# Kernel optimization log

Hardware: AMD Instinct MI355X
Metric: run time of the kernel (lower is better)

## Reference

```python
import jax, jax.numpy as jnp
import numpy as np

B, T, F, H, O = 16384, 128, 9, 128, 12


def setup_inputs() -> dict:
    key = jax.random.key(0)
    ks = jax.random.split(key, 14)
    s = 1.0 / np.sqrt(H)
    u = lambda k, shp: jax.random.uniform(k, shp, jnp.float32, -s, s)
    return {
        "x": jax.random.normal(ks[0], (B, T, F), jnp.float32),
        "W_in": u(ks[1], (H, F)), "b_in": u(ks[2], (H,)),
        "Wih0": u(ks[3], (4 * H, H)), "Whh0": u(ks[4], (4 * H, H)),
        "bih0": u(ks[5], (4 * H,)), "bhh0": u(ks[6], (4 * H,)),
        "Wih1": u(ks[7], (4 * H, H)), "Whh1": u(ks[8], (4 * H, H)),
        "bih1": u(ks[9], (4 * H,)), "bhh1": u(ks[10], (4 * H,)),
        "W_out": u(ks[11], (O, H)), "b_out": u(ks[12], (O,)),
    }


def _cell(h, c, xp, Wih, Whh, bih, bhh):
    # PyTorch LSTM gate order: i, f, g, o
    g = xp @ Wih.T + bih + h @ Whh.T + bhh  # [B, 4H]
    i, f, gg, o = jnp.split(g, 4, axis=-1)
    c = jax.nn.sigmoid(f) * c + jax.nn.sigmoid(i) * jnp.tanh(gg)
    h = jax.nn.sigmoid(o) * jnp.tanh(c)
    return h, c


def reference(x, W_in, b_in, Wih0, Whh0, bih0, bhh0, Wih1, Whh1, bih1, bhh1, W_out, b_out):
    # input projection, all timesteps at once: [B, T, H] -> scan over time
    xp = jnp.einsum('btf,hf->tbh', x, W_in) + b_in
    b = x.shape[0]
    zeros = jnp.zeros((b, H), x.dtype)
    carry0 = (zeros, zeros, zeros, zeros)  # h0, c0, h1, c1

    def step(carry, xt):
        h0, c0, h1, c1 = carry
        h0, c0 = _cell(h0, c0, xt, Wih0, Whh0, bih0, bhh0)
        h1, c1 = _cell(h1, c1, h0, Wih1, Whh1, bih1, bhh1)
        return (h0, c0, h1, c1), None

    (h0, c0, h1, c1), _ = jax.lax.scan(step, carry0, xp)
    # torch forward returns only the LAST step's output: out(h1) with softmax over dim=1
    return jax.nn.softmax(h1 @ W_out.T + b_out, axis=1)
```

## Files before the change

kernel.cpp:

```cpp
#include <hip/hip_runtime.h>
#include <hip/hip_bf16.h>
#include <stdint.h>
#include <stddef.h>

#define T_STEPS 128
#define F_IN 9
#define HID 128
#define OUT_N 12
#define XROW (T_STEPS * F_IN)
#define BATCH 16384

typedef __attribute__((ext_vector_type(8))) short bf16x8;
typedef __attribute__((ext_vector_type(4))) float f32x4;

#define MFMA16(a, b, c) __builtin_amdgcn_mfma_f32_16x16x32_bf16((a), (b), (c), 0, 0, 0)

__device__ __forceinline__ short f2bf(float f) {
  union { float f; uint32_t u; } v; v.f = f;
  return (short)((v.u + 0x7fffu + ((v.u >> 16) & 1u)) >> 16);
}
__device__ __forceinline__ short f2bf_hw(float f) {
  __hip_bfloat16 h = __float2bfloat16(f);
  union { __hip_bfloat16 h; short s; } u; u.h = h;
  return u.s;
}
__device__ __forceinline__ float frcp(float x) { return __builtin_amdgcn_rcpf(x); }
__device__ __forceinline__ float fexp2(float x) { return __builtin_amdgcn_exp2f(x); }
__device__ __forceinline__ float tanh_f(float x) {
  return 1.0f - 2.0f * frcp(1.0f + fexp2(2.8853900817779268f * x));
}

__global__ void prep_x(const float* __restrict__ x, short* __restrict__ xbf) {
  int idx = blockIdx.x * blockDim.x + threadIdx.x;
  int row = idx & (BATCH - 1), t = idx >> 14;
  const float* xp = x + (size_t)row * XROW + t * F_IN;
  short v[16];
#pragma unroll
  for (int j = 0; j < F_IN; ++j) v[j] = f2bf(xp[j]);
#pragma unroll
  for (int j = F_IN; j < 16; ++j) v[j] = 0;
  int4* dst = (int4*)(xbf + (size_t)idx * 16);
  dst[0] = ((const int4*)v)[0];
  dst[1] = ((const int4*)v)[1];
}

__global__ void prep_w0x(const float* __restrict__ W_in, const float* __restrict__ b_in,
                         const float* __restrict__ Wih0, const float* __restrict__ bih0,
                         const float* __restrict__ bhh0, const float* __restrict__ bih1,
                         const float* __restrict__ bhh1,
                         short* __restrict__ w0xf, float* __restrict__ b0x, float* __restrict__ b1) {
  int tid = threadIdx.x;
  int nt = tid >> 4, hl = tid & 15;
  int w = nt >> 2, g = nt & 3;
  int n = g * 128 + w * 16 + hl;
  float wacc[F_IN];
#pragma unroll
  for (int f = 0; f < F_IN; ++f) wacc[f] = 0.f;
  float bacc = 0.f;
  for (int h = 0; h < HID; ++h) {
    float wv = Wih0[n * HID + h];
    bacc += wv * b_in[h];
#pragma unroll
    for (int f = 0; f < F_IN; ++f) wacc[f] += wv * W_in[h * F_IN + f];
  }
  b0x[n] = bacc + bih0[n] + bhh0[n];
  b1[n] = bih1[n] + bhh1[n];
#pragma unroll
  for (int k = 0; k < 32; ++k) {
    int quad = k >> 3, j = k & 7;
    w0xf[((w * 4 + g) * 64 + quad * 16 + hl) * 8 + j] = (k < F_IN) ? f2bf(wacc[k]) : (short)0;
  }
}

__global__ void prep_wrec(const float* __restrict__ Whh0, const float* __restrict__ Wih1,
                          const float* __restrict__ Whh1,
                          short* __restrict__ whh0f, short* __restrict__ w1f) {
  int gt = blockIdx.x * blockDim.x + threadIdx.x;
  if (gt < 2048) {
    int kt = gt >> 9, rr = gt & 511;
    int nt = rr >> 4, hl = rr & 15;
    int w = nt >> 2, g = nt & 3;
    int n = g * 128 + w * 16 + hl;
#pragma unroll
    for (int k = 0; k < 32; ++k) {
      int quad = k >> 3, j = k & 7;
      whh0f[((w * 16 + kt * 4 + g) * 64 + quad * 16 + hl) * 8 + j] =
          f2bf(Whh0[n * HID + kt * 32 + k]);
    }
  } else {
    int g2 = gt - 2048;
    int kt = g2 >> 9, rr = g2 & 511;
    int nt = rr >> 4, hl = rr & 15;
    int w = nt >> 2, g = nt & 3;
    int n = g * 128 + w * 16 + hl;
#pragma unroll
    for (int k = 0; k < 32; ++k) {
      int quad = k >> 3, j = k & 7;
      int kg = kt * 32 + k;
      float v = (kg < HID) ? Wih1[n * HID + kg] : Whh1[n * HID + kg - HID];
      w1f[((w * 32 + kt * 4 + g) * 64 + quad * 16 + hl) * 8 + j] = f2bf(v);
    }
  }
}

__device__ __forceinline__ void lstm_step(
    int t, const short* __restrict__ xpl, const short* __restrict__ wp0,
    const short* __restrict__ wph, const short* __restrict__ wp1,
    const float* sb0, const float* sb1, float* c0, float* c1,
    const short* h0r, short* h0w, const short* h1r, short* h1w,
    int lane, int wr_off, int quad) {
  const f32x4 z4 = {0.f, 0.f, 0.f, 0.f};
  const short* xt = xpl + (size_t)t * 262144;
  bf16x8 xf[2];
#pragma unroll
  for (int mt = 0; mt < 2; ++mt) {
    bf16x8 v = {0, 0, 0, 0, 0, 0, 0, 0};
    if (quad < 2) v = *(const bf16x8*)(xt + mt * 256);
    xf[mt] = v;
  }
  f32x4 acc1[2][4];
  {
    const short* wb = wp1;
    bf16x8 b0_ = *(const bf16x8*)(wb);
    bf16x8 b1_ = *(const bf16x8*)(wb + 512);
    bf16x8 b2_ = *(const bf16x8*)(wb + 1024);
    bf16x8 b3_ = *(const bf16x8*)(wb + 1536);
#pragma unroll
    for (int mt = 0; mt < 2; ++mt) {
      bf16x8 af = *(const bf16x8*)(h0r + ((mt * 4 + 0) * 64 + lane) * 8);
      acc1[mt][0] = MFMA16(af, b0_, z4);
      acc1[mt][1] = MFMA16(af, b1_, z4);
      acc1[mt][2] = MFMA16(af, b2_, z4);
      acc1[mt][3] = MFMA16(af, b3_, z4);
    }
  }
#pragma clang loop unroll_count(3)
  for (int kt = 1; kt < 4; ++kt) {
    const short* wb = wp1 + kt * 2048;
    bf16x8 b0_ = *(const bf16x8*)(wb);
    bf16x8 b1_ = *(const bf16x8*)(wb + 512);
    bf16x8 b2_ = *(const bf16x8*)(wb + 1024);
    bf16x8 b3_ = *(const bf16x8*)(wb + 1536);
#pragma unroll
    for (int mt = 0; mt < 2; ++mt) {
      bf16x8 af = *(const bf16x8*)(h0r + ((mt * 4 + kt) * 64 + lane) * 8);
      acc1[mt][0] = MFMA16(af, b0_, acc1[mt][0]);
      acc1[mt][1] = MFMA16(af, b1_, acc1[mt][1]);
      acc1[mt][2] = MFMA16(af, b2_, acc1[mt][2]);
      acc1[mt][3] = MFMA16(af, b3_, acc1[mt][3]);
    }
  }
#pragma clang loop unroll_count(2)
  for (int kt = 0; kt < 4; ++kt) {
    const short* wb = wp1 + (kt + 4) * 2048;
    bf16x8 b0_ = *(const bf16x8*)(wb);
    bf16x8 b1_ = *(const bf16x8*)(wb + 512);
    bf16x8 b2_ = *(const bf16x8*)(wb + 1024);
    bf16x8 b3_ = *(const bf16x8*)(wb + 1536);
#pragma unroll
    for (int mt = 0; mt < 2; ++mt) {
      bf16x8 af = *(const bf16x8*)(h1r + ((mt * 4 + kt) * 64 + lane) * 8);
      acc1[mt][0] = MFMA16(af, b0_, acc1[mt][0]);
      acc1[mt][1] = MFMA16(af, b1_, acc1[mt][1]);
      acc1[mt][2] = MFMA16(af, b2_, acc1[mt][2]);
      acc1[mt][3] = MFMA16(af, b3_, acc1[mt][3]);
    }
  }
#pragma unroll
  for (int mt = 0; mt < 2; ++mt)
#pragma unroll
    for (int r = 0; r < 4; ++r) {
      float gi = frcp(1.0f + fexp2(fmaf(-1.4426950408889634f, acc1[mt][0][r], sb1[0])));
      float gf = frcp(1.0f + fexp2(fmaf(-1.4426950408889634f, acc1[mt][1][r], sb1[1])));
      float gg = 1.0f - 2.0f * frcp(1.0f + fexp2(fmaf(2.8853900817779268f, acc1[mt][2][r], sb1[2])));
      float go = frcp(1.0f + fexp2(fmaf(-1.4426950408889634f, acc1[mt][3][r], sb1[3])));
      float cn = gf * c1[mt * 4 + r] + gi * gg;
      c1[mt * 4 + r] = cn;
      float hn = go * tanh_f(cn);
      h1w[mt * 2048 + r * 8 + wr_off] = f2bf_hw(hn);
    }
  f32x4 acc0[2][4];
  {
    bf16x8 b0_ = *(const bf16x8*)(wp0);
    bf16x8 b1_ = *(const bf16x8*)(wp0 + 512);
    bf16x8 b2_ = *(const bf16x8*)(wp0 + 1024);
    bf16x8 b3_ = *(const bf16x8*)(wp0 + 1536);
#pragma unroll
    for (int mt = 0; mt < 2; ++mt) {
      acc0[mt][0] = MFMA16(xf[mt], b0_, z4);
      acc0[mt][1] = MFMA16(xf[mt], b1_, z4);
      acc0[mt][2] = MFMA16(xf[mt], b2_, z4);
      acc0[mt][3] = MFMA16(xf[mt], b3_, z4);
    }
  }
#pragma clang loop unroll_count(2)
  for (int kt = 0; kt < 4; ++kt) {
    const short* wb = wph + kt * 2048;
    bf16x8 b0_ = *(const bf16x8*)(wb);
    bf16x8 b1_ = *(const bf16x8*)(wb + 512);
    bf16x8 b2_ = *(const bf16x8*)(wb + 1024);
    bf16x8 b3_ = *(const bf16x8*)(wb + 1536);
#pragma unroll
    for (int mt = 0; mt < 2; ++mt) {
      bf16x8 af = *(const bf16x8*)(h0r + ((mt * 4 + kt) * 64 + lane) * 8);
      acc0[mt][0] = MFMA16(af, b0_, acc0[mt][0]);
      acc0[mt][1] = MFMA16(af, b1_, acc0[mt][1]);
      acc0[mt][2] = MFMA16(af, b2_, acc0[mt][2]);
      acc0[mt][3] = MFMA16(af, b3_, acc0[mt][3]);
    }
  }
#pragma unroll
  for (int mt = 0; mt < 2; ++mt)
#pragma unroll
    for (int r = 0; r < 4; ++r) {
      float gi = frcp(1.0f + fexp2(fmaf(-1.4426950408889634f, acc0[mt][0][r], sb0[0])));
      float gf = frcp(1.0f + fexp2(fmaf(-1.4426950408889634f, acc0[mt][1][r], sb0[1])));
      float gg = 1.0f - 2.0f * frcp(1.0f + fexp2(fmaf(2.8853900817779268f, acc0[mt][2][r], sb0[2])));
      float go = frcp(1.0f + fexp2(fmaf(-1.4426950408889634f, acc0[mt][3][r], sb0[3])));
      float cn = gf * c0[mt * 4 + r] + gi * gg;
      c0[mt * 4 + r] = cn;
      float hn = go * tanh_f(cn);
      h0w[mt * 2048 + r * 8 + wr_off] = f2bf_hw(hn);
    }
  __syncthreads();
}

__global__ void __launch_bounds__(512)
lstm_main(const short* __restrict__ xbf, const short* __restrict__ w0xf,
          const short* __restrict__ whh0f, const short* __restrict__ w1f,
          const float* __restrict__ b0x, const float* __restrict__ b1,
          const float* __restrict__ Wout, const float* __restrict__ bout,
          float* __restrict__ out) {
  __shared__ short h0a[4096], h0b[4096], h1a[4096], h1b[4096];
  __shared__ float h1fp[32 * HID];
  __shared__ float lg[32 * OUT_N];
  __shared__ int gov[2688];

  const int tid = threadIdx.x;
  const int w = tid >> 6, lane = tid & 63;
  const int quad = lane >> 4, c = lane & 15;
  const int rowbase = blockIdx.x * 32;

  {
    for (int i = tid; i < 2048; i += 512) {
      ((int*)h0a)[i] = 0; ((int*)h0b)[i] = 0; ((int*)h1a)[i] = 0; ((int*)h1b)[i] = 0;
    }
    if (tid < 64) ((volatile int*)gov)[tid] = 0;
  }

  const short* wp0 = w0xf + (w * 4) * 512 + lane * 8;
  const short* wph = whh0f + (w * 16) * 512 + lane * 8;
  const short* wp1 = w1f + (w * 32) * 512 + lane * 8;

  const short* xpl = xbf + ((size_t)(rowbase + c) << 4) + ((quad & 1) << 3);

  float sb0[4], sb1[4];
#pragma unroll
  for (int g = 0; g < 4; ++g) {
    int n = g * 128 + w * 16 + c;
    float bv0 = b0x[n], bv1 = b1[n];
    sb0[g] = (g == 2) ? 2.8853900817779268f * bv0 : -1.4426950408889634f * bv0;
    sb1[g] = (g == 2) ? 2.8853900817779268f * bv1 : -1.4426950408889634f * bv1;
  }

  const int kt_w = w >> 1;
  const int klocal = ((w & 1) << 4) + c;
  const int quadA = klocal >> 3;
  const int jA = klocal & 7;
  const int wr_off = (kt_w * 64 + quadA * 16 + quad * 4) * 8 + jA;

  float c0[8], c1[8];
#pragma unroll
  for (int i = 0; i < 8; ++i) { c0[i] = 0.f; c1[i] = 0.f; }

  const f32x4 z4 = {0.f, 0.f, 0.f, 0.f};

  __syncthreads();

  {
    bf16x8 xf[2];
#pragma unroll
    for (int mt = 0; mt < 2; ++mt) {
      bf16x8 v = {0, 0, 0, 0, 0, 0, 0, 0};
      if (quad < 2) v = *(const bf16x8*)(xpl + mt * 256);
      xf[mt] = v;
    }
    f32x4 acc[2][4];
    {
      bf16x8 b0_ = *(const bf16x8*)(wp0);
      bf16x8 b1_ = *(const bf16x8*)(wp0 + 512);
      bf16x8 b2_ = *(const bf16x8*)(wp0 + 1024);
      bf16x8 b3_ = *(const bf16x8*)(wp0 + 1536);
#pragma unroll
      for (int mt = 0; mt < 2; ++mt) {
        acc[mt][0] = MFMA16(xf[mt], b0_, z4);
        acc[mt][1] = MFMA16(xf[mt], b1_, z4);
        acc[mt][2] = MFMA16(xf[mt], b2_, z4);
        acc[mt][3] = MFMA16(xf[mt], b3_, z4);
      }
    }
#pragma unroll
    for (int mt = 0; mt < 2; ++mt)
#pragma unroll
      for (int r = 0; r < 4; ++r) {
        float gi = frcp(1.0f + fexp2(fmaf(-1.4426950408889634f, acc[mt][0][r], sb0[0])));
        float gf = frcp(1.0f + fexp2(fmaf(-1.4426950408889634f, acc[mt][1][r], sb0[1])));
        float gg = 1.0f - 2.0f * frcp(1.0f + fexp2(fmaf(2.8853900817779268f, acc[mt][2][r], sb0[2])));
        float go = frcp(1.0f + fexp2(fmaf(-1.4426950408889634f, acc[mt][3][r], sb0[3])));
        float cn = gi * gg;
        c0[mt * 4 + r] = cn;
        float hn = go * tanh_f(cn);
        h0a[mt * 2048 + r * 8 + wr_off] = f2bf_hw(hn);
      }
  }
  __syncthreads();

#pragma clang loop unroll(disable)
  for (int t = 1; t < 127; t += 2) {
    lstm_step(t,     xpl, wp0, wph, wp1, sb0, sb1, c0, c1, h0a, h0b, h1a, h1b, lane, wr_off, quad);
    lstm_step(t + 1, xpl, wp0, wph, wp1, sb0, sb1, c0, c1, h0b, h0a, h1b, h1a, lane, wr_off, quad);
  }
  lstm_step(127, xpl, wp0, wph, wp1, sb0, sb1, c0, c1, h0a, h0b, h1a, h1b, lane, wr_off, quad);

  {
    f32x4 acc[2][4];
    {
      const short* wb = wp1;
      bf16x8 b0_ = *(const bf16x8*)(wb);
      bf16x8 b1_ = *(const bf16x8*)(wb + 512);
      bf16x8 b2_ = *(const bf16x8*)(wb + 1024);
      bf16x8 b3_ = *(const bf16x8*)(wb + 1536);
#pragma unroll
      for (int mt = 0; mt < 2; ++mt) {
        bf16x8 af = *(const bf16x8*)(h0b + ((mt * 4 + 0) * 64 + lane) * 8);
        acc[mt][0] = MFMA16(af, b0_, z4);
        acc[mt][1] = MFMA16(af, b1_, z4);
        acc[mt][2] = MFMA16(af, b2_, z4);
        acc[mt][3] = MFMA16(af, b3_, z4);
      }
    }
#pragma unroll
    for (int kt = 1; kt < 4; ++kt) {
      const short* wb = wp1 + kt * 2048;
      bf16x8 b0_ = *(const bf16x8*)(wb);
      bf16x8 b1_ = *(const bf16x8*)(wb + 512);
      bf16x8 b2_ = *(const bf16x8*)(wb + 1024);
      bf16x8 b3_ = *(const bf16x8*)(wb + 1536);
#pragma unroll
      for (int mt = 0; mt < 2; ++mt) {
        bf16x8 af = *(const bf16x8*)(h0b + ((mt * 4 + kt) * 64 + lane) * 8);
        acc[mt][0] = MFMA16(af, b0_, acc[mt][0]);
        acc[mt][1] = MFMA16(af, b1_, acc[mt][1]);
        acc[mt][2] = MFMA16(af, b2_, acc[mt][2]);
        acc[mt][3] = MFMA16(af, b3_, acc[mt][3]);
      }
    }
#pragma unroll
    for (int kt = 0; kt < 4; ++kt) {
      const short* wb = wp1 + (kt + 4) * 2048;
      bf16x8 b0_ = *(const bf16x8*)(wb);
      bf16x8 b1_ = *(const bf16x8*)(wb + 512);
      bf16x8 b2_ = *(const bf16x8*)(wb + 1024);
      bf16x8 b3_ = *(const bf16x8*)(wb + 1536);
#pragma unroll
      for (int mt = 0; mt < 2; ++mt) {
        bf16x8 af = *(const bf16x8*)(h1b + ((mt * 4 + kt) * 64 + lane) * 8);
        acc[mt][0] = MFMA16(af, b0_, acc[mt][0]);
        acc[mt][1] = MFMA16(af, b1_, acc[mt][1]);
        acc[mt][2] = MFMA16(af, b2_, acc[mt][2]);
        acc[mt][3] = MFMA16(af, b3_, acc[mt][3]);
      }
    }
#pragma unroll
    for (int mt = 0; mt < 2; ++mt)
#pragma unroll
      for (int r = 0; r < 4; ++r) {
        float gi = frcp(1.0f + fexp2(fmaf(-1.4426950408889634f, acc[mt][0][r], sb1[0])));
        float gf = frcp(1.0f + fexp2(fmaf(-1.4426950408889634f, acc[mt][1][r], sb1[1])));
        float gg = 1.0f - 2.0f * frcp(1.0f + fexp2(fmaf(2.8853900817779268f, acc[mt][2][r], sb1[2])));
        float go = frcp(1.0f + fexp2(fmaf(-1.4426950408889634f, acc[mt][3][r], sb1[3])));
        float cn = gf * c1[mt * 4 + r] + gi * gg;
        float hn = go * tanh_f(cn);
        h1fp[(mt * 16 + quad * 4 + r) * HID + w * 16 + c] = hn;
      }
  }
  __syncthreads();

  {
    int row = tid >> 4, og = tid & 15;
    for (int oc = og; oc < OUT_N; oc += 16) {
      float s = bout[oc];
      const float* wo = Wout + oc * HID;
      const float* hr = h1fp + row * HID;
#pragma unroll 8
      for (int k = 0; k < HID; ++k) s += hr[k] * wo[k];
      lg[row * OUT_N + oc] = s;
    }
  }
  __syncthreads();
  if (tid < 32) {
    int row = tid;
    float m = lg[row * OUT_N];
#pragma unroll
    for (int oc = 1; oc < OUT_N; ++oc) m = fmaxf(m, lg[row * OUT_N + oc]);
    float e[OUT_N];
    float s = 0.f;
#pragma unroll
    for (int oc = 0; oc < OUT_N; ++oc) {
      e[oc] = __expf(lg[row * OUT_N + oc] - m);
      s += e[oc];
    }
    float inv = 1.0f / s;
    float* orow = out + (size_t)(rowbase + row) * OUT_N;
#pragma unroll
    for (int oc = 0; oc < OUT_N; ++oc) orow[oc] = e[oc] * inv;
  }
}

extern "C" void kernel_launch(void* const* d_in, const int* in_sizes, int n_in,
                              void* d_out, int out_size, void* d_ws, size_t ws_size,
                              hipStream_t stream) {
  const float* x    = (const float*)d_in[0];
  const float* W_in = (const float*)d_in[1];
  const float* b_in = (const float*)d_in[2];
  const float* Wih0 = (const float*)d_in[3];
  const float* Whh0 = (const float*)d_in[4];
  const float* bih0 = (const float*)d_in[5];
  const float* bhh0 = (const float*)d_in[6];
  const float* Wih1 = (const float*)d_in[7];
  const float* Whh1 = (const float*)d_in[8];
  const float* bih1 = (const float*)d_in[9];
  const float* bhh1 = (const float*)d_in[10];
  const float* Wout = (const float*)d_in[11];
  const float* bout = (const float*)d_in[12];
  float* out = (float*)d_out;

  short* w0xf  = (short*)d_ws;
  short* whh0f = w0xf + 16384;
  short* w1f   = whh0f + 65536;
  float* b0x   = (float*)(w1f + 131072);
  float* b1    = b0x + 512;
  short* xbf   = (short*)(b1 + 512);

  prep_x<<<(BATCH * T_STEPS) / 256, 256, 0, stream>>>(x, xbf);
  prep_w0x<<<1, 512, 0, stream>>>(W_in, b_in, Wih0, bih0, bhh0, bih1, bhh1, w0xf, b0x, b1);
  prep_wrec<<<12, 512, 0, stream>>>(Whh0, Wih1, Whh1, whh0f, w1f);
  lstm_main<<<512, 512, 0, stream>>>(xbf, w0xf, whh0f, w1f, b0x, b1, Wout, bout, out);
}
```

Measured before the change: 1.212 ms.

## Double rows per block to 64 and move cell state into LDS

Each block now handles 64 batch rows instead of 32 (4 M-tiles per warp), so each recurrent weight fragment loaded per step feeds twice as many MFMAs. The grid is halved to 256 blocks. To hold register pressure down with the larger accumulators, the LSTM cell states c0/c1 move from registers into shared memory and are read and written as float4 per thread each step. The risks are fewer blocks than CUs on the device, more LDS per block, and extra LDS traffic on every step.

```diff
diff --git a/kernel.cpp b/kernel.cpp
--- a/kernel.cpp
+++ b/kernel.cpp
@@ -106,19 +106,13 @@
 __device__ __forceinline__ void lstm_step(
     int t, const short* __restrict__ xpl, const short* __restrict__ wp0,
     const short* __restrict__ wph, const short* __restrict__ wp1,
-    const float* sb0, const float* sb1, float* c0, float* c1,
+    const float* sb0, const float* sb1, float* c0buf, float* c1buf,
     const short* h0r, short* h0w, const short* h1r, short* h1w,
-    int lane, int wr_off, int quad) {
+    int tid, int lane, int wr_off, int quad) {
   const f32x4 z4 = {0.f, 0.f, 0.f, 0.f};
   const short* xt = xpl + (size_t)t * 262144;
-  bf16x8 xf[2];
-#pragma unroll
-  for (int mt = 0; mt < 2; ++mt) {
-    bf16x8 v = {0, 0, 0, 0, 0, 0, 0, 0};
-    if (quad < 2) v = *(const bf16x8*)(xt + mt * 256);
-    xf[mt] = v;
-  }
-  f32x4 acc1[2][4];
+
+  f32x4 acc1[4][4];
   {
     const short* wb = wp1;
     bf16x8 b0_ = *(const bf16x8*)(wb);
@@ -126,7 +120,7 @@
     bf16x8 b2_ = *(const bf16x8*)(wb + 1024);
     bf16x8 b3_ = *(const bf16x8*)(wb + 1536);
 #pragma unroll
-    for (int mt = 0; mt < 2; ++mt) {
+    for (int mt = 0; mt < 4; ++mt) {
       bf16x8 af = *(const bf16x8*)(h0r + ((mt * 4 + 0) * 64 + lane) * 8);
       acc1[mt][0] = MFMA16(af, b0_, z4);
       acc1[mt][1] = MFMA16(af, b1_, z4);
@@ -142,7 +136,7 @@
     bf16x8 b2_ = *(const bf16x8*)(wb + 1024);
     bf16x8 b3_ = *(const bf16x8*)(wb + 1536);
 #pragma unroll
-    for (int mt = 0; mt < 2; ++mt) {
+    for (int mt = 0; mt < 4; ++mt) {
       bf16x8 af = *(const bf16x8*)(h0r + ((mt * 4 + kt) * 64 + lane) * 8);
       acc1[mt][0] = MFMA16(af, b0_, acc1[mt][0]);
       acc1[mt][1] = MFMA16(af, b1_, acc1[mt][1]);
@@ -158,7 +152,7 @@
     bf16x8 b2_ = *(const bf16x8*)(wb + 1024);
     bf16x8 b3_ = *(const bf16x8*)(wb + 1536);
 #pragma unroll
-    for (int mt = 0; mt < 2; ++mt) {
+    for (int mt = 0; mt < 4; ++mt) {
       bf16x8 af = *(const bf16x8*)(h1r + ((mt * 4 + kt) * 64 + lane) * 8);
       acc1[mt][0] = MFMA16(af, b0_, acc1[mt][0]);
       acc1[mt][1] = MFMA16(af, b1_, acc1[mt][1]);
@@ -167,30 +161,35 @@
     }
   }
 #pragma unroll
-  for (int mt = 0; mt < 2; ++mt)
+  for (int mt = 0; mt < 4; ++mt) {
+    f32x4 cp = *(const f32x4*)(c1buf + 4 * (mt * 512 + tid));
+    f32x4 cn;
 #pragma unroll
     for (int r = 0; r < 4; ++r) {
       float gi = frcp(1.0f + fexp2(fmaf(-1.4426950408889634f, acc1[mt][0][r], sb1[0])));
       float gf = frcp(1.0f + fexp2(fmaf(-1.4426950408889634f, acc1[mt][1][r], sb1[1])));
       float gg = 1.0f - 2.0f * frcp(1.0f + fexp2(fmaf(2.8853900817779268f, acc1[mt][2][r], sb1[2])));
       float go = frcp(1.0f + fexp2(fmaf(-1.4426950408889634f, acc1[mt][3][r], sb1[3])));
-      float cn = gf * c1[mt * 4 + r] + gi * gg;
-      c1[mt * 4 + r] = cn;
-      float hn = go * tanh_f(cn);
+      cn[r] = gf * cp[r] + gi * gg;
+      float hn = go * tanh_f(cn[r]);
       h1w[mt * 2048 + r * 8 + wr_off] = f2bf_hw(hn);
     }
-  f32x4 acc0[2][4];
+    *(f32x4*)(c1buf + 4 * (mt * 512 + tid)) = cn;
+  }
+  f32x4 acc0[4][4];
   {
     bf16x8 b0_ = *(const bf16x8*)(wp0);
     bf16x8 b1_ = *(const bf16x8*)(wp0 + 512);
     bf16x8 b2_ = *(const bf16x8*)(wp0 + 1024);
     bf16x8 b3_ = *(const bf16x8*)(wp0 + 1536);
 #pragma unroll
-    for (int mt = 0; mt < 2; ++mt) {
-      acc0[mt][0] = MFMA16(xf[mt], b0_, z4);
-      acc0[mt][1] = MFMA16(xf[mt], b1_, z4);
-      acc0[mt][2] = MFMA16(xf[mt], b2_, z4);
-      acc0[mt][3] = MFMA16(xf[mt], b3_, z4);
+    for (int mt = 0; mt < 4; ++mt) {
+      bf16x8 xf = {0, 0, 0, 0, 0, 0, 0, 0};
+      if (quad < 2) xf = *(const bf16x8*)(xt + mt * 256);
+      acc0[mt][0] = MFMA16(xf, b0_, z4);
+      acc0[mt][1] = MFMA16(xf, b1_, z4);
+      acc0[mt][2] = MFMA16(xf, b2_, z4);
+      acc0[mt][3] = MFMA16(xf, b3_, z4);
     }
   }
 #pragma clang loop unroll_count(2)
@@ -201,7 +200,7 @@
     bf16x8 b2_ = *(const bf16x8*)(wb + 1024);
     bf16x8 b3_ = *(const bf16x8*)(wb + 1536);
 #pragma unroll
-    for (int mt = 0; mt < 2; ++mt) {
+    for (int mt = 0; mt < 4; ++mt) {
       bf16x8 af = *(const bf16x8*)(h0r + ((mt * 4 + kt) * 64 + lane) * 8);
       acc0[mt][0] = MFMA16(af, b0_, acc0[mt][0]);
       acc0[mt][1] = MFMA16(af, b1_, acc0[mt][1]);
@@ -210,18 +209,21 @@
     }
   }
 #pragma unroll
-  for (int mt = 0; mt < 2; ++mt)
+  for (int mt = 0; mt < 4; ++mt) {
+    f32x4 cp = *(const f32x4*)(c0buf + 4 * (mt * 512 + tid));
+    f32x4 cn;
 #pragma unroll
     for (int r = 0; r < 4; ++r) {
       float gi = frcp(1.0f + fexp2(fmaf(-1.4426950408889634f, acc0[mt][0][r], sb0[0])));
       float gf = frcp(1.0f + fexp2(fmaf(-1.4426950408889634f, acc0[mt][1][r], sb0[1])));
       float gg = 1.0f - 2.0f * frcp(1.0f + fexp2(fmaf(2.8853900817779268f, acc0[mt][2][r], sb0[2])));
       float go = frcp(1.0f + fexp2(fmaf(-1.4426950408889634f, acc0[mt][3][r], sb0[3])));
-      float cn = gf * c0[mt * 4 + r] + gi * gg;
-      c0[mt * 4 + r] = cn;
-      float hn = go * tanh_f(cn);
+      cn[r] = gf * cp[r] + gi * gg;
+      float hn = go * tanh_f(cn[r]);
       h0w[mt * 2048 + r * 8 + wr_off] = f2bf_hw(hn);
     }
+    *(f32x4*)(c0buf + 4 * (mt * 512 + tid)) = cn;
+  }
   __syncthreads();
 }
 
@@ -231,21 +233,21 @@
           const float* __restrict__ b0x, const float* __restrict__ b1,
           const float* __restrict__ Wout, const float* __restrict__ bout,
           float* __restrict__ out) {
-  __shared__ short h0a[4096], h0b[4096], h1a[4096], h1b[4096];
-  __shared__ float h1fp[32 * HID];
-  __shared__ float lg[32 * OUT_N];
-  __shared__ int gov[2688];
+  __shared__ short h0a[8192], h0b[8192], h1a[8192], h1b[8192];
+  __shared__ float h1fp_c0[64 * HID];
+  __shared__ float c1buf[64 * HID];
+  __shared__ float lg[64 * OUT_N];
 
   const int tid = threadIdx.x;
   const int w = tid >> 6, lane = tid & 63;
   const int quad = lane >> 4, c = lane & 15;
-  const int rowbase = blockIdx.x * 32;
-
-  {
-    for (int i = tid; i < 2048; i += 512) {
+  const int rowbase = blockIdx.x * 64;
+
+  {
+    for (int i = tid; i < 4096; i += 512) {
       ((int*)h0a)[i] = 0; ((int*)h0b)[i] = 0; ((int*)h1a)[i] = 0; ((int*)h1b)[i] = 0;
     }
-    if (tid < 64) ((volatile int*)gov)[tid] = 0;
+    for (int i = tid; i < 8192; i += 512) { h1fp_c0[i] = 0.f; c1buf[i] = 0.f; }
   }
 
   const short* wp0 = w0xf + (w * 4) * 512 + lane * 8;
@@ -269,61 +271,56 @@
   const int jA = klocal & 7;
   const int wr_off = (kt_w * 64 + quadA * 16 + quad * 4) * 8 + jA;
 
-  float c0[8], c1[8];
-#pragma unroll
-  for (int i = 0; i < 8; ++i) { c0[i] = 0.f; c1[i] = 0.f; }
-
   const f32x4 z4 = {0.f, 0.f, 0.f, 0.f};
 
   __syncthreads();
 
   {
-    bf16x8 xf[2];
-#pragma unroll
-    for (int mt = 0; mt < 2; ++mt) {
-      bf16x8 v = {0, 0, 0, 0, 0, 0, 0, 0};
-      if (quad < 2) v = *(const bf16x8*)(xpl + mt * 256);
-      xf[mt] = v;
-    }
-    f32x4 acc[2][4];
+    f32x4 acc[4][4];
     {
       bf16x8 b0_ = *(const bf16x8*)(wp0);
       bf16x8 b1_ = *(const bf16x8*)(wp0 + 512);
       bf16x8 b2_ = *(const bf16x8*)(wp0 + 1024);
       bf16x8 b3_ = *(const bf16x8*)(wp0 + 1536);
 #pragma unroll
-      for (int mt = 0; mt < 2; ++mt) {
-        acc[mt][0] = MFMA16(xf[mt], b0_, z4);
-        acc[mt][1] = MFMA16(xf[mt], b1_, z4);
-        acc[mt][2] = MFMA16(xf[mt], b2_, z4);
-        acc[mt][3] = MFMA16(xf[mt], b3_, z4);
-      }
-    }
-#pragma unroll
-    for (int mt = 0; mt < 2; ++mt)
+      for (int mt = 0; mt < 4; ++mt) {
+        bf16x8 xf = {0, 0, 0, 0, 0, 0, 0, 0};
+        if (quad < 2) xf = *(const bf16x8*)(xpl + mt * 256);
+        acc[mt][0] = MFMA16(xf, b0_, z4);
+        acc[mt][1] = MFMA16(xf, b1_, z4);
+        acc[mt][2] = MFMA16(xf, b2_, z4);
+        acc[mt][3] = MFMA16(xf, b3_, z4);
+      }
+    }
+#pragma unroll
+    for (int mt = 0; mt < 4; ++mt) {
+      f32x4 cn;
 #pragma unroll
       for (int r = 0; r < 4; ++r) {
         float gi = frcp(1.0f + fexp2(fmaf(-1.4426950408889634f, acc[mt][0][r], sb0[0])));
-        float gf = frcp(1.0f + fexp2(fmaf(-1.4426950408889634f, acc[mt][1][r], sb0[1])));
         float gg = 1.0f - 2.0f * frcp(1.0f + fexp2(fmaf(2.8853900817779268f, acc[mt][2][r], sb0[2])));
         float go = frcp(1.0f + fexp2(fmaf(-1.4426950408889634f, acc[mt][3][r], sb0[3])));
-        float cn = gi * gg;
-        c0[mt * 4 + r] = cn;
-        float hn = go * tanh_f(cn);
+        cn[r] = gi * gg;
+        float hn = go * tanh_f(cn[r]);
         h0a[mt * 2048 + r * 8 + wr_off] = f2bf_hw(hn);
       }
+      *(f32x4*)(h1fp_c0 + 4 * (mt * 512 + tid)) = cn;
+    }
   }
   __syncthreads();
 
 #pragma clang loop unroll(disable)
   for (int t = 1; t < 127; t += 2) {
-    lstm_step(t,     xpl, wp0, wph, wp1, sb0, sb1, c0, c1, h0a, h0b, h1a, h1b, lane, wr_off, quad);
-    lstm_step(t + 1, xpl, wp0, wph, wp1, sb0, sb1, c0, c1, h0b, h0a, h1b, h1a, lane, wr_off, quad);
-  }
-  lstm_step(127, xpl, wp0, wph, wp1, sb0, sb1, c0, c1, h0a, h0b, h1a, h1b, lane, wr_off, quad);
-
-  {
-    f32x4 acc[2][4];
+    lstm_step(t,     xpl, wp0, wph, wp1, sb0, sb1, h1fp_c0, c1buf, h0a, h0b, h1a, h1b,
+              tid, lane, wr_off, quad);
+    lstm_step(t + 1, xpl, wp0, wph, wp1, sb0, sb1, h1fp_c0, c1buf, h0b, h0a, h1b, h1a,
+              tid, lane, wr_off, quad);
+  }
+  lstm_step(127, xpl, wp0, wph, wp1, sb0, sb1, h1fp_c0, c1buf, h0a, h0b, h1a, h1b,
+            tid, lane, wr_off, quad);
+
+  {
+    f32x4 acc[4][4];
     {
       const short* wb = wp1;
       bf16x8 b0_ = *(const bf16x8*)(wb);
@@ -331,7 +328,7 @@
       bf16x8 b2_ = *(const bf16x8*)(wb + 1024);
       bf16x8 b3_ = *(const bf16x8*)(wb + 1536);
 #pragma unroll
-      for (int mt = 0; mt < 2; ++mt) {
+      for (int mt = 0; mt < 4; ++mt) {
         bf16x8 af = *(const bf16x8*)(h0b + ((mt * 4 + 0) * 64 + lane) * 8);
         acc[mt][0] = MFMA16(af, b0_, z4);
         acc[mt][1] = MFMA16(af, b1_, z4);
@@ -347,7 +344,7 @@
       bf16x8 b2_ = *(const bf16x8*)(wb + 1024);
       bf16x8 b3_ = *(const bf16x8*)(wb + 1536);
 #pragma unroll
-      for (int mt = 0; mt < 2; ++mt) {
+      for (int mt = 0; mt < 4; ++mt) {
         bf16x8 af = *(const bf16x8*)(h0b + ((mt * 4 + kt) * 64 + lane) * 8);
         acc[mt][0] = MFMA16(af, b0_, acc[mt][0]);
         acc[mt][1] = MFMA16(af, b1_, acc[mt][1]);
@@ -363,7 +360,7 @@
       bf16x8 b2_ = *(const bf16x8*)(wb + 1024);
       bf16x8 b3_ = *(const bf16x8*)(wb + 1536);
 #pragma unroll
-      for (int mt = 0; mt < 2; ++mt) {
+      for (int mt = 0; mt < 4; ++mt) {
         bf16x8 af = *(const bf16x8*)(h1b + ((mt * 4 + kt) * 64 + lane) * 8);
         acc[mt][0] = MFMA16(af, b0_, acc[mt][0]);
         acc[mt][1] = MFMA16(af, b1_, acc[mt][1]);
@@ -371,34 +368,37 @@
         acc[mt][3] = MFMA16(af, b3_, acc[mt][3]);
       }
     }
-#pragma unroll
-    for (int mt = 0; mt < 2; ++mt)
+    __syncthreads();
+#pragma unroll
+    for (int mt = 0; mt < 4; ++mt) {
+      f32x4 cp = *(const f32x4*)(c1buf + 4 * (mt * 512 + tid));
 #pragma unroll
       for (int r = 0; r < 4; ++r) {
         float gi = frcp(1.0f + fexp2(fmaf(-1.4426950408889634f, acc[mt][0][r], sb1[0])));
         float gf = frcp(1.0f + fexp2(fmaf(-1.4426950408889634f, acc[mt][1][r], sb1[1])));
         float gg = 1.0f - 2.0f * frcp(1.0f + fexp2(fmaf(2.8853900817779268f, acc[mt][2][r], sb1[2])));
         float go = frcp(1.0f + fexp2(fmaf(-1.4426950408889634f, acc[mt][3][r], sb1[3])));
-        float cn = gf * c1[mt * 4 + r] + gi * gg;
+        float cn = gf * cp[r] + gi * gg;
         float hn = go * tanh_f(cn);
-        h1fp[(mt * 16 + quad * 4 + r) * HID + w * 16 + c] = hn;
-      }
+        h1fp_c0[(mt * 16 + quad * 4 + r) * HID + w * 16 + c] = hn;
+      }
+    }
   }
   __syncthreads();
 
   {
-    int row = tid >> 4, og = tid & 15;
-    for (int oc = og; oc < OUT_N; oc += 16) {
+    int row = tid >> 3, og = tid & 7;
+    for (int oc = og; oc < OUT_N; oc += 8) {
       float s = bout[oc];
       const float* wo = Wout + oc * HID;
-      const float* hr = h1fp + row * HID;
+      const float* hr = h1fp_c0 + row * HID;
 #pragma unroll 8
       for (int k = 0; k < HID; ++k) s += hr[k] * wo[k];
       lg[row * OUT_N + oc] = s;
     }
   }
   __syncthreads();
-  if (tid < 32) {
+  if (tid < 64) {
     int row = tid;
     float m = lg[row * OUT_N];
 #pragma unroll
@@ -445,5 +445,5 @@
   prep_x<<<(BATCH * T_STEPS) / 256, 256, 0, stream>>>(x, xbf);
   prep_w0x<<<1, 512, 0, stream>>>(W_in, b_in, Wih0, bih0, bhh0, bih1, bhh1, w0xf, b0x, b1);
   prep_wrec<<<12, 512, 0, stream>>>(Whh0, Wih1, Whh1, whh0f, w1f);
-  lstm_main<<<512, 512, 0, stream>>>(xbf, w0xf, whh0f, w1f, b0x, b1, Wout, bout, out);
-}
+  lstm_main<<<256, 512, 0, stream>>>(xbf, w0xf, whh0f, w1f, b0x, b1, Wout, bout, out);
+}
```

Measured after the change: 1.184 ms, median of 2. 1.02x faster.
